# Optimization experiments

Hardware: AMD Instinct MI355X
Metric: run time of the kernel (lower is better)

## Reference

```python
import jax, jax.numpy as jnp
import numpy as np

DIM = 1024
HEADS = 16
DIM_HEAD = 64
INNER = HEADS * DIM_HEAD
SEQ = 4096
BATCH = 1


def setup_inputs() -> dict:
    key = jax.random.key(0)
    ks = jax.random.split(key, 6)
    s = 0.02
    return {
        "x": jax.random.normal(ks[0], (BATCH, SEQ, DIM), dtype=jnp.float32),
        "Wq": jax.random.normal(ks[1], (DIM, INNER), dtype=jnp.float32) * s,
        "Wk": jax.random.normal(ks[2], (DIM, INNER), dtype=jnp.float32) * s,
        "Wv": jax.random.normal(ks[3], (DIM, INNER), dtype=jnp.float32) * s,
        "Wo": jax.random.normal(ks[4], (INNER, DIM), dtype=jnp.float32) * s,
        "bo": jax.random.normal(ks[5], (DIM,), dtype=jnp.float32) * s,
    }


def reference(x, Wq, Wk, Wv, Wo, bo):
    b, n, _ = x.shape
    beta = 1.0 / jnp.sqrt(jnp.float32(DIM_HEAD))
    # project and split heads: [b, n, inner] -> [b, h, n, d]
    def split_heads(t):
        return t.reshape(b, n, HEADS, DIM_HEAD).transpose(0, 2, 1, 3)
    q = split_heads(x @ Wq)
    k = split_heads(x @ Wk)
    v = split_heads(x @ Wv)
    # scaled scores [b, h, n, n]
    scores = jnp.einsum('bhid,bhjd->bhij', q * beta, k)
    mask_value = -jnp.finfo(scores.dtype).max
    causal = jnp.triu(jnp.ones((n, n), dtype=bool), k=1)
    scores = jnp.where(causal, mask_value, scores)
    attn = jax.nn.softmax(scores, axis=-1)
    out = jnp.einsum('bhij,bhjd->bhid', attn, v)
    out = out.transpose(0, 2, 1, 3).reshape(b, n, INNER)
    # output projection (dropout is identity in eval)
    return out @ Wo + bo
```

## Files before the change

### kernel.cpp

```cpp
#include <hip/hip_runtime.h>
#include <hip/hip_bf16.h>
#include <stdint.h>
#include <math.h>

#define SEQ 4096
#define DIM 1024
#define NHEADS 16
#define DHEAD 64
#define INNER 1024

typedef __hip_bfloat16 bf16;
typedef __attribute__((ext_vector_type(8))) short short8;
typedef __attribute__((ext_vector_type(4))) float floatx4;

__device__ __forceinline__ void gll16(const bf16* g, bf16* l) {
    __builtin_amdgcn_global_load_lds(
        (const __attribute__((address_space(1))) unsigned int*)g,
        (__attribute__((address_space(3))) unsigned int*)l,
        16, 0, 0);
}

__device__ __forceinline__ unsigned short f2bf_bits(float f) {
    bf16 h = __float2bfloat16(f);
    return *reinterpret_cast<unsigned short*>(&h);
}

__device__ __forceinline__ uint2 pack4bf(float a, float b, float c, float d) {
    __hip_bfloat162 lo = __float22bfloat162_rn(float2{a, b});
    __hip_bfloat162 hi = __float22bfloat162_rn(float2{c, d});
    uint2 r;
    r.x = *reinterpret_cast<unsigned*>(&lo);
    r.y = *reinterpret_cast<unsigned*>(&hi);
    return r;
}

__global__ __launch_bounds__(256) void convert_x_kernel(const float* __restrict__ x,
                                                        bf16* __restrict__ xb) {
    int i = (blockIdx.x * 256 + threadIdx.x) * 4;
    float4 f = *reinterpret_cast<const float4*>(x + i);
    unsigned long long p = (unsigned long long)f2bf_bits(f.x)
                         | ((unsigned long long)f2bf_bits(f.y) << 16)
                         | ((unsigned long long)f2bf_bits(f.z) << 32)
                         | ((unsigned long long)f2bf_bits(f.w) << 48);
    *reinterpret_cast<unsigned long long*>(xb + i) = p;
}

__global__ __launch_bounds__(256) void transpose_w_kernel(
        const float* __restrict__ W0, const float* __restrict__ W1,
        const float* __restrict__ W2, const float* __restrict__ W3,
        bf16* __restrict__ T0, bf16* __restrict__ T1,
        bf16* __restrict__ T2, bf16* __restrict__ T3) {
    const float* W; bf16* T;
    switch (blockIdx.z) {
        case 0:  W = W0; T = T0; break;
        case 1:  W = W1; T = T1; break;
        case 2:  W = W2; T = T2; break;
        default: W = W3; T = T3; break;
    }
    __shared__ float tile[32][33];
    int k0 = blockIdx.x * 32, n0 = blockIdx.y * 32;
    int tx = threadIdx.x, ty = threadIdx.y;
    #pragma unroll
    for (int i = 0; i < 4; i++)
        tile[ty + 8 * i][tx] = W[(size_t)(k0 + ty + 8 * i) * 1024 + n0 + tx];
    __syncthreads();
    #pragma unroll
    for (int i = 0; i < 4; i++)
        T[(size_t)(n0 + ty + 8 * i) * 1024 + k0 + tx] = __float2bfloat16(tile[tx][ty + 8 * i]);
}

__global__ __launch_bounds__(256) void transpose_v_kernel(const bf16* __restrict__ Vh,
                                                          bf16* __restrict__ Vt) {
    __shared__ bf16 tile[32][33];
    int h = blockIdx.z;
    int n0 = blockIdx.x * 32, d0 = blockIdx.y * 32;
    int tx = threadIdx.x, ty = threadIdx.y;
    const bf16* src = Vh + (size_t)h * SEQ * DHEAD;
    bf16* dst = Vt + (size_t)h * DHEAD * SEQ;
    #pragma unroll
    for (int i = 0; i < 4; i++)
        tile[ty + 8 * i][tx] = src[(size_t)(n0 + ty + 8 * i) * DHEAD + d0 + tx];
    __syncthreads();
    #pragma unroll
    for (int i = 0; i < 4; i++)
        dst[(size_t)(d0 + ty + 8 * i) * SEQ + n0 + tx] = tile[tx][ty + 8 * i];
}

__device__ __forceinline__ void gemm128_body(const bf16* __restrict__ A,
                                             const bf16* __restrict__ Bt,
                                             int m0, int n0, floatx4 acc[4][4]) {
    __shared__ __align__(16) bf16 As[8192];
    __shared__ __align__(16) bf16 Bs[8192];
    const int tid = threadIdx.x;
    const int wave = tid >> 6;
    const int lane = tid & 63;
    const int l15 = lane & 15;
    const int quad = lane >> 4;

    #pragma unroll
    for (int i = 0; i < 4; i++)
        #pragma unroll
        for (int j = 0; j < 4; j++)
            acc[i][j] = (floatx4){0.f, 0.f, 0.f, 0.f};

    for (int k0 = 0; k0 < 1024; k0 += 64) {
        __syncthreads();
        #pragma unroll
        for (int j = 0; j < 4; j++) {
            int t = wave * 4 + j;
            int row = (t >> 1) * 16 + l15;
            int kb = (t & 1) * 32 + quad * 8;
            gll16(A + (size_t)(m0 + row) * 1024 + k0 + kb, &As[t * 512]);
            gll16(Bt + (size_t)(n0 + row) * 1024 + k0 + kb, &Bs[t * 512]);
        }
        __syncthreads();
        #pragma unroll
        for (int ks = 0; ks < 2; ks++) {
            short8 af[4], bfr[4];
            #pragma unroll
            for (int i = 0; i < 4; i++)
                af[i] = *reinterpret_cast<const short8*>(
                    &As[((((wave >> 1) * 4 + i) * 2 + ks) * 512) + lane * 8]);
            #pragma unroll
            for (int j = 0; j < 4; j++)
                bfr[j] = *reinterpret_cast<const short8*>(
                    &Bs[((((wave & 1) * 4 + j) * 2 + ks) * 512) + lane * 8]);
            #pragma unroll
            for (int i = 0; i < 4; i++)
                #pragma unroll
                for (int j = 0; j < 4; j++)
                    acc[i][j] = __builtin_amdgcn_mfma_f32_16x16x32_bf16(af[i], bfr[j], acc[i][j], 0, 0, 0);
        }
    }
}

__global__ __launch_bounds__(256) void qkv_gemm_kernel(
        const bf16* __restrict__ xb,
        const bf16* __restrict__ Wqt, const bf16* __restrict__ Wkt, const bf16* __restrict__ Wvt,
        bf16* __restrict__ Qh, bf16* __restrict__ Kh, bf16* __restrict__ Vh) {
    const bf16* Bt; bf16* O; float scale = 1.0f;
    if (blockIdx.z == 0)      { Bt = Wqt; O = Qh; scale = 0.125f * 1.4426950408889634f; }
    else if (blockIdx.z == 1) { Bt = Wkt; O = Kh; }
    else                      { Bt = Wvt; O = Vh; }
    int n0 = blockIdx.x * 128, m0 = blockIdx.y * 128;
    floatx4 acc[4][4];
    gemm128_body(xb, Bt, m0, n0, acc);

    const int tid = threadIdx.x, wave = tid >> 6, lane = tid & 63;
    const int l15 = lane & 15, quad = lane >> 4;
    const int wm = (wave >> 1) * 64, wn = (wave & 1) * 64;
    #pragma unroll
    for (int i = 0; i < 4; i++)
        #pragma unroll
        for (int j = 0; j < 4; j++) {
            int col = n0 + wn + j * 16 + l15;
            int h = col >> 6, d = col & 63;
            #pragma unroll
            for (int r = 0; r < 4; r++) {
                int row = m0 + wm + i * 16 + quad * 4 + r;
                O[((size_t)h * SEQ + row) * DHEAD + d] = __float2bfloat16(acc[i][j][r] * scale);
            }
        }
}

__global__ __launch_bounds__(256) void out_gemm_kernel(
        const bf16* __restrict__ Oa, const bf16* __restrict__ Wot,
        const float* __restrict__ bo, float* __restrict__ out) {
    int n0 = blockIdx.x * 128, m0 = blockIdx.y * 128;
    floatx4 acc[4][4];
    gemm128_body(Oa, Wot, m0, n0, acc);

    const int tid = threadIdx.x, wave = tid >> 6, lane = tid & 63;
    const int l15 = lane & 15, quad = lane >> 4;
    const int wm = (wave >> 1) * 64, wn = (wave & 1) * 64;
    #pragma unroll
    for (int i = 0; i < 4; i++)
        #pragma unroll
        for (int j = 0; j < 4; j++) {
            int col = n0 + wn + j * 16 + l15;
            float b = bo[col];
            #pragma unroll
            for (int r = 0; r < 4; r++) {
                int row = m0 + wm + i * 16 + quad * 4 + r;
                out[(size_t)row * DIM + col] = acc[i][j][r] + b;
            }
        }
}

__global__ __launch_bounds__(256, 2) void attention_kernel(
        const bf16* __restrict__ Qh, const bf16* __restrict__ Kh,
        const bf16* __restrict__ Vt, bf16* __restrict__ Oa) {
    __shared__ __align__(16) bf16 Ksh[8192];
    __shared__ __align__(16) bf16 Vsh[8192];
    __shared__ __align__(16) bf16 Ps[4][4096];
    const int tid = threadIdx.x, wave = tid >> 6, lane = tid & 63;
    const int l15 = lane & 15, quad = lane >> 4;
    const int id = blockIdx.x;
    const int head = id & 15;
    const int rid = id >> 4;
    const int qt = (id < 256) ? (31 - rid) : (rid - 16);
    const int qw = qt * 128 + wave * 32;
    const size_t hoff = (size_t)head * SEQ * DHEAD;
    const bf16* Qb = Qh + hoff;
    const bf16* Kb = Kh + hoff;
    const bf16* Vb = Vt + hoff;

    short8 bq[2][2];
    #pragma unroll
    for (int g = 0; g < 2; g++)
        #pragma unroll
        for (int s = 0; s < 2; s++)
            bq[g][s] = *reinterpret_cast<const short8*>(
                Qb + (size_t)(qw + g * 16 + l15) * DHEAD + s * 32 + quad * 8);

    floatx4 acc_o[2][4];
    #pragma unroll
    for (int g = 0; g < 2; g++)
        #pragma unroll
        for (int c = 0; c < 4; c++) acc_o[g][c] = (floatx4){0.f, 0.f, 0.f, 0.f};
    float l_part[2] = {0.f, 0.f};

    const int ntiles = qt + 1;
    for (int kt = 0; kt < ntiles; kt++) {
        const int kbase = kt * 128;
        __syncthreads();
        #pragma unroll
        for (int j = 0; j < 4; j++) {
            int t = wave * 4 + j;
            gll16(Kb + (size_t)(kbase + (t >> 1) * 16 + l15) * DHEAD + (t & 1) * 32 + quad * 8,
                  &Ksh[t * 512]);
            gll16(Vb + (size_t)((t >> 2) * 16 + l15) * SEQ + kbase + (t & 3) * 32 + quad * 8,
                  &Vsh[t * 512]);
        }
        __syncthreads();

        floatx4 st[2][8];
        #pragma unroll
        for (int g = 0; g < 2; g++)
            #pragma unroll
            for (int c = 0; c < 8; c++) st[g][c] = (floatx4){0.f, 0.f, 0.f, 0.f};
        #pragma unroll
        for (int c = 0; c < 8; c++) {
            short8 ak0 = *reinterpret_cast<const short8*>(&Ksh[(c * 2 + 0) * 512 + lane * 8]);
            short8 ak1 = *reinterpret_cast<const short8*>(&Ksh[(c * 2 + 1) * 512 + lane * 8]);
            st[0][c] = __builtin_amdgcn_mfma_f32_16x16x32_bf16(ak0, bq[0][0], st[0][c], 0, 0, 0);
            st[0][c] = __builtin_amdgcn_mfma_f32_16x16x32_bf16(ak1, bq[0][1], st[0][c], 0, 0, 0);
            st[1][c] = __builtin_amdgcn_mfma_f32_16x16x32_bf16(ak0, bq[1][0], st[1][c], 0, 0, 0);
            st[1][c] = __builtin_amdgcn_mfma_f32_16x16x32_bf16(ak1, bq[1][1], st[1][c], 0, 0, 0);
        }
        #pragma unroll
        for (int g = 0; g < 2; g++) {
            if (kbase + 127 > qw + g * 16) {
                int base0 = kbase + quad * 4 - (qw + g * 16) - l15;
                #pragma unroll
                for (int c = 0; c < 8; c++) {
                    int base = base0 + c * 16;
                    #pragma unroll
                    for (int r = 0; r < 4; r++)
                        if (base + r > 0) st[g][c][r] = -1e30f;
                }
            }
        }
        #pragma unroll
        for (int g = 0; g < 2; g++)
            #pragma unroll
            for (int c = 0; c < 8; c++) {
                float p0 = exp2f(st[g][c][0]);
                float p1 = exp2f(st[g][c][1]);
                float p2 = exp2f(st[g][c][2]);
                float p3 = exp2f(st[g][c][3]);
                l_part[g] += (p0 + p1) + (p2 + p3);
                int elem = (g * 4 + (c >> 1)) * 512
                         + (l15 + 16 * ((c & 1) * 2 + (quad >> 1))) * 8 + (quad & 1) * 4;
                *reinterpret_cast<uint2*>(&Ps[wave][elem]) = pack4bf(p0, p1, p2, p3);
            }
        #pragma unroll
        for (int s = 0; s < 4; s++) {
            short8 bp0 = *reinterpret_cast<const short8*>(&Ps[wave][(s) * 512 + lane * 8]);
            short8 bp1 = *reinterpret_cast<const short8*>(&Ps[wave][(4 + s) * 512 + lane * 8]);
            #pragma unroll
            for (int c = 0; c < 4; c++) {
                short8 av = *reinterpret_cast<const short8*>(&Vsh[(c * 4 + s) * 512 + lane * 8]);
                acc_o[0][c] = __builtin_amdgcn_mfma_f32_16x16x32_bf16(av, bp0, acc_o[0][c], 0, 0, 0);
                acc_o[1][c] = __builtin_amdgcn_mfma_f32_16x16x32_bf16(av, bp1, acc_o[1][c], 0, 0, 0);
            }
        }
    }
    #pragma unroll
    for (int g = 0; g < 2; g++) {
        float l = l_part[g];
        l += __shfl_xor(l, 16, 64);
        l += __shfl_xor(l, 32, 64);
        float rcp = 1.0f / l;
        const int q = qw + g * 16 + l15;
        #pragma unroll
        for (int c = 0; c < 4; c++) {
            uint2 v = pack4bf(acc_o[g][c][0] * rcp, acc_o[g][c][1] * rcp,
                              acc_o[g][c][2] * rcp, acc_o[g][c][3] * rcp);
            *reinterpret_cast<uint2*>(Oa + (size_t)q * INNER + head * DHEAD + c * 16 + quad * 4) = v;
        }
    }
}

extern "C" void kernel_launch(void* const* d_in, const int* in_sizes, int n_in,
                              void* d_out, int out_size, void* d_ws, size_t ws_size,
                              hipStream_t stream) {
    const float* x  = (const float*)d_in[0];
    const float* Wq = (const float*)d_in[1];
    const float* Wk = (const float*)d_in[2];
    const float* Wv = (const float*)d_in[3];
    const float* Wo = (const float*)d_in[4];
    const float* bo = (const float*)d_in[5];
    float* out = (float*)d_out;

    char* ws = (char*)d_ws;
    size_t off = 0;
    bf16* xb  = (bf16*)(ws + off); off += (size_t)SEQ * DIM * 2;
    bf16* Wqt = (bf16*)(ws + off); off += (size_t)DIM * INNER * 2;
    bf16* Wkt = (bf16*)(ws + off); off += (size_t)DIM * INNER * 2;
    bf16* Wvt = (bf16*)(ws + off); off += (size_t)DIM * INNER * 2;
    bf16* Wot = (bf16*)(ws + off); off += (size_t)INNER * DIM * 2;
    bf16* Qh  = (bf16*)(ws + off); off += (size_t)NHEADS * SEQ * DHEAD * 2;
    bf16* Kh  = (bf16*)(ws + off); off += (size_t)NHEADS * SEQ * DHEAD * 2;
    bf16* Vh  = (bf16*)(ws + off); off += (size_t)NHEADS * SEQ * DHEAD * 2;
    bf16* Vtr = (bf16*)(ws + off); off += (size_t)NHEADS * DHEAD * SEQ * 2;
    bf16* Oa  = (bf16*)(ws + off); off += (size_t)SEQ * INNER * 2;

    convert_x_kernel<<<(SEQ * DIM) / 1024, 256, 0, stream>>>(x, xb);
    transpose_w_kernel<<<dim3(32, 32, 4), dim3(32, 8), 0, stream>>>(Wq, Wk, Wv, Wo,
                                                                    Wqt, Wkt, Wvt, Wot);
    qkv_gemm_kernel<<<dim3(8, 32, 3), 256, 0, stream>>>(xb, Wqt, Wkt, Wvt, Qh, Kh, Vh);
    transpose_v_kernel<<<dim3(SEQ / 32, DHEAD / 32, NHEADS), dim3(32, 8), 0, stream>>>(Vh, Vtr);
    attention_kernel<<<512, 256, 0, stream>>>(Qh, Kh, Vtr, Oa);
    out_gemm_kernel<<<dim3(8, 32), 256, 0, stream>>>(Oa, Wot, bo, out);
}
```

Baseline: 281.3 us.

## Split attention into single-wave blocks reading K/V directly from global memory

The attention kernel goes from 256-thread blocks (four waves sharing LDS-staged K/V tiles for 128 queries) to 64-thread single-wave blocks of 32 queries each, launched as 2048 blocks with a serpentine causal tile order. K and V fragments are loaded straight from global memory into registers, which removes the LDS staging and both block barriers per tile. The aim is finer causal load balancing and no synchronization stalls, at the cost of losing K/V reuse across waves: each wave now fetches K/V itself, raising global/L2 traffic roughly fourfold, and the loads are no longer overlapped with compute.

```diff
diff --git a/kernel.cpp b/kernel.cpp
--- a/kernel.cpp
+++ b/kernel.cpp
@@ -187,19 +187,18 @@
         }
 }
 
-__global__ __launch_bounds__(256, 2) void attention_kernel(
+__global__ __launch_bounds__(64, 2) void attention_kernel(
         const bf16* __restrict__ Qh, const bf16* __restrict__ Kh,
         const bf16* __restrict__ Vt, bf16* __restrict__ Oa) {
-    __shared__ __align__(16) bf16 Ksh[8192];
-    __shared__ __align__(16) bf16 Vsh[8192];
-    __shared__ __align__(16) bf16 Ps[4][4096];
-    const int tid = threadIdx.x, wave = tid >> 6, lane = tid & 63;
+    __shared__ __align__(16) bf16 Ps[4096];
+    const int lane = threadIdx.x & 63;
     const int l15 = lane & 15, quad = lane >> 4;
     const int id = blockIdx.x;
     const int head = id & 15;
     const int rid = id >> 4;
-    const int qt = (id < 256) ? (31 - rid) : (rid - 16);
-    const int qw = qt * 128 + wave * 32;
+    const int low = rid & 15, hi = rid >> 4;
+    const int qt = hi * 16 + ((hi & 1) ? (15 - low) : low);
+    const int qw = qt * 32;
     const size_t hoff = (size_t)head * SEQ * DHEAD;
     const bf16* Qb = Qh + hoff;
     const bf16* Kb = Kh + hoff;
@@ -220,29 +219,22 @@
         for (int c = 0; c < 4; c++) acc_o[g][c] = (floatx4){0.f, 0.f, 0.f, 0.f};
     float l_part[2] = {0.f, 0.f};
 
-    const int ntiles = qt + 1;
+    const bf16* kp0 = Kb + l15 * DHEAD + quad * 8;
+    const bf16* vp0 = Vb + (size_t)l15 * SEQ + quad * 8;
+
+    const int ntiles = (qt >> 2) + 1;
     for (int kt = 0; kt < ntiles; kt++) {
         const int kbase = kt * 128;
-        __syncthreads();
-        #pragma unroll
-        for (int j = 0; j < 4; j++) {
-            int t = wave * 4 + j;
-            gll16(Kb + (size_t)(kbase + (t >> 1) * 16 + l15) * DHEAD + (t & 1) * 32 + quad * 8,
-                  &Ksh[t * 512]);
-            gll16(Vb + (size_t)((t >> 2) * 16 + l15) * SEQ + kbase + (t & 3) * 32 + quad * 8,
-                  &Vsh[t * 512]);
-        }
-        __syncthreads();
-
         floatx4 st[2][8];
         #pragma unroll
         for (int g = 0; g < 2; g++)
             #pragma unroll
             for (int c = 0; c < 8; c++) st[g][c] = (floatx4){0.f, 0.f, 0.f, 0.f};
+        const bf16* kp = kp0 + kbase * DHEAD;
         #pragma unroll
         for (int c = 0; c < 8; c++) {
-            short8 ak0 = *reinterpret_cast<const short8*>(&Ksh[(c * 2 + 0) * 512 + lane * 8]);
-            short8 ak1 = *reinterpret_cast<const short8*>(&Ksh[(c * 2 + 1) * 512 + lane * 8]);
+            short8 ak0 = *reinterpret_cast<const short8*>(kp + c * (16 * DHEAD));
+            short8 ak1 = *reinterpret_cast<const short8*>(kp + c * (16 * DHEAD) + 32);
             st[0][c] = __builtin_amdgcn_mfma_f32_16x16x32_bf16(ak0, bq[0][0], st[0][c], 0, 0, 0);
             st[0][c] = __builtin_amdgcn_mfma_f32_16x16x32_bf16(ak1, bq[0][1], st[0][c], 0, 0, 0);
             st[1][c] = __builtin_amdgcn_mfma_f32_16x16x32_bf16(ak0, bq[1][0], st[1][c], 0, 0, 0);
@@ -272,15 +264,17 @@
                 l_part[g] += (p0 + p1) + (p2 + p3);
                 int elem = (g * 4 + (c >> 1)) * 512
                          + (l15 + 16 * ((c & 1) * 2 + (quad >> 1))) * 8 + (quad & 1) * 4;
-                *reinterpret_cast<uint2*>(&Ps[wave][elem]) = pack4bf(p0, p1, p2, p3);
-            }
+                *reinterpret_cast<uint2*>(&Ps[elem]) = pack4bf(p0, p1, p2, p3);
+            }
+        const bf16* vp = vp0 + kbase;
         #pragma unroll
         for (int s = 0; s < 4; s++) {
-            short8 bp0 = *reinterpret_cast<const short8*>(&Ps[wave][(s) * 512 + lane * 8]);
-            short8 bp1 = *reinterpret_cast<const short8*>(&Ps[wave][(4 + s) * 512 + lane * 8]);
+            short8 bp0 = *reinterpret_cast<const short8*>(&Ps[(s) * 512 + lane * 8]);
+            short8 bp1 = *reinterpret_cast<const short8*>(&Ps[(4 + s) * 512 + lane * 8]);
             #pragma unroll
             for (int c = 0; c < 4; c++) {
-                short8 av = *reinterpret_cast<const short8*>(&Vsh[(c * 4 + s) * 512 + lane * 8]);
+                short8 av = *reinterpret_cast<const short8*>(
+                    vp + (size_t)c * (16 * SEQ) + s * 32);
                 acc_o[0][c] = __builtin_amdgcn_mfma_f32_16x16x32_bf16(av, bp0, acc_o[0][c], 0, 0, 0);
                 acc_o[1][c] = __builtin_amdgcn_mfma_f32_16x16x32_bf16(av, bp1, acc_o[1][c], 0, 0, 0);
             }
@@ -331,6 +325,6 @@
                                                                     Wqt, Wkt, Wvt, Wot);
     qkv_gemm_kernel<<<dim3(8, 32, 3), 256, 0, stream>>>(xb, Wqt, Wkt, Wvt, Qh, Kh, Vh);
     transpose_v_kernel<<<dim3(SEQ / 32, DHEAD / 32, NHEADS), dim3(32, 8), 0, stream>>>(Vh, Vtr);
-    attention_kernel<<<512, 256, 0, stream>>>(Qh, Kh, Vtr, Oa);
+    attention_kernel<<<2048, 64, 0, stream>>>(Qh, Kh, Vtr, Oa);
     out_gemm_kernel<<<dim3(8, 32), 256, 0, stream>>>(Oa, Wot, bo, out);
 }
```

After: 372.4 us. 32.4% more time.
